# Performance work log

Measured on AMD Instinct MI355X. Metric: run time of the kernel, lower is better.

The kernel has to match this reference:

```python
import jax, jax.numpy as jnp
import numpy as np

GRAPH_SIZE = 96
ROWS = 5
COLS = 4
BATCH = 2048


def setup_inputs() -> dict:
    key = jax.random.key(0)
    k1, k2 = jax.random.split(key)
    x = jax.random.normal(k1, (BATCH, GRAPH_SIZE, GRAPH_SIZE), dtype=jnp.float32)
    # coef: nn.Parameter zeros -> kaiming_normal_, i.e. N(0, sqrt(2/fan_in)), fan_in=COLS
    coef = jax.random.normal(k2, (ROWS, COLS), dtype=jnp.float32) * np.float32(np.sqrt(2.0 / COLS))
    return {"x": x, "coef": coef}


def _acoef(x, coef):
    """Batched version of ACoef.forward.

    Per sample: t_i = trace(x^(i+2)) for i in [0, rows); scalar out =
    sum_{i,j} coef[i,j] * t_i^(j+1) / (G*G)^(i+j+1).
    """
    rows, cols = coef.shape
    G = x.shape[-1]
    xr = x.reshape(-1, G, G)  # [B, G, G]
    a = jnp.matmul(xr, xr)    # x^2 == a_series[0]
    traces = []
    for i in range(rows):
        traces.append(jnp.einsum('bii->b', a))  # trace(x^(i+2))
        if i < rows - 1:
            a = jnp.matmul(xr, a)  # advance to x^(i+3)
    t = jnp.stack(traces, axis=1)  # [B, rows]
    numel = jnp.float32(G * G)
    jexp = jnp.arange(1, cols + 1, dtype=jnp.float32)  # j+1
    iexp = jnp.arange(rows, dtype=jnp.float32)         # i
    denom = numel ** (iexp[:, None] + jexp[None, :])   # numel^(i+j+1), [rows, cols]
    ret = (t[:, :, None] ** jexp[None, None, :]) / denom  # [B, rows, cols]
    return jnp.sum(coef[None, :, :] * ret, axis=(1, 2))   # [B]


def reference(x, coef):
    return _acoef(x, coef)
```

## Files before the change

### kernel.cpp

```cpp
#include <hip/hip_runtime.h>
#include <stdint.h>

#define G 96
#define GS (G*G)
#define ST 104
#define ARR (G*ST)
#define NT 256

typedef short bf16x8  __attribute__((ext_vector_type(8)));
typedef short short4v __attribute__((ext_vector_type(4)));
typedef float f32x4   __attribute__((ext_vector_type(4)));

__device__ __forceinline__ short f2bf(float f) {
  uint32_t u = __builtin_bit_cast(uint32_t, f);
  u += 0x7FFFu + ((u >> 16) & 1u);
  return (short)(u >> 16);
}
__device__ __forceinline__ float bf2f(short s) {
  uint32_t u = ((uint32_t)(uint16_t)s) << 16;
  return __builtin_bit_cast(float, u);
}

__device__ __forceinline__ void mm_phase(const short* __restrict__ P,
                                         const short* __restrict__ Q,
                                         int wm, int wn, int lr, int lq,
                                         f32x4 acc[3][3]) {
  #pragma unroll
  for (int ks = 0; ks < 3; ++ks) {
    const int k0 = ks*32 + lq*8;
    bf16x8 af[3], bg[3];
    #pragma unroll
    for (int i = 0; i < 3; ++i)
      af[i] = *reinterpret_cast<const bf16x8*>(&P[(wm + i*16 + lr)*ST + k0]);
    #pragma unroll
    for (int j = 0; j < 3; ++j)
      bg[j] = *reinterpret_cast<const bf16x8*>(&Q[(wn + j*16 + lr)*ST + k0]);
    #pragma unroll
    for (int i = 0; i < 3; ++i)
      #pragma unroll
      for (int j = 0; j < 3; ++j)
        acc[i][j] = __builtin_amdgcn_mfma_f32_16x16x32_bf16(af[i], bg[j], acc[i][j], 0, 0, 0);
  }
}

__global__ __launch_bounds__(NT, 4) void acoef_kernel(
    const float* __restrict__ x, const float* __restrict__ coef,
    float* __restrict__ out) {
  __shared__ short sm[2*ARR];
  __shared__ float red[4][8];

  short* X  = sm;
  short* R1 = sm + ARR;

  const int tid  = threadIdx.x;
  const int b    = blockIdx.x;
  const int lane = tid & 63;
  const int w    = tid >> 6;
  const int wm   = (w >> 1) * 48;
  const int wn   = (w & 1)  * 48;
  const int lr   = lane & 15;
  const int lq   = lane >> 4;
  const int cr0  = lq * 4;

  const float* xg = x + (size_t)b * GS;
  #pragma unroll
  for (int it = 0; it < 9; ++it) {
    int f = tid + it*NT;
    float4 v = reinterpret_cast<const float4*>(xg)[f];
    int row = f / 24, c4 = (f - row*24) * 4;
    short4v sv = {f2bf(v.x), f2bf(v.y), f2bf(v.z), f2bf(v.w)};
    *reinterpret_cast<short4v*>(&X[row*ST + c4]) = sv;
  }
  __syncthreads();

  #pragma unroll
  for (int it = 0; it < 9; ++it) {
    int u  = tid + it*NT;
    int r2 = u % 96, cb = (u / 96) * 4;
    short4v sv = { X[(cb+0)*ST + r2], X[(cb+1)*ST + r2],
                   X[(cb+2)*ST + r2], X[(cb+3)*ST + r2] };
    *reinterpret_cast<short4v*>(&R1[r2*ST + cb]) = sv;
  }
  __syncthreads();

  f32x4 acc[3][3];
  #pragma unroll
  for (int i=0;i<3;i++)
    #pragma unroll
    for (int j=0;j<3;j++) acc[i][j] = (f32x4){0.f,0.f,0.f,0.f};
  mm_phase(X, R1, wm, wn, lr, lq, acc);

  float t0 = 0.f;
  #pragma unroll
  for (int i = 0; i < 3; ++i)
    #pragma unroll
    for (int j = 0; j < 3; ++j) {
      const int row0 = wm + i*16 + cr0, col = wn + j*16 + lr;
      #pragma unroll
      for (int r = 0; r < 4; ++r)
        if (row0 + r == col) t0 += acc[i][j][r];
    }
  __syncthreads();

  #pragma unroll
  for (int i = 0; i < 3; ++i)
    #pragma unroll
    for (int j = 0; j < 3; ++j) {
      const int row0 = wm + i*16 + cr0, col = wn + j*16 + lr;
      short4v sv = {f2bf(acc[i][j][0]), f2bf(acc[i][j][1]),
                    f2bf(acc[i][j][2]), f2bf(acc[i][j][3])};
      *reinterpret_cast<short4v*>(&R1[col*ST + row0]) = sv;
    }
  __syncthreads();

  f32x4 a2[3][3];
  #pragma unroll
  for (int i=0;i<3;i++)
    #pragma unroll
    for (int j=0;j<3;j++) a2[i][j] = (f32x4){0.f,0.f,0.f,0.f};
  mm_phase(R1, X, wm, wn, lr, lq, a2);

  float t1=0.f, t2=0.f, t3=0.f, t4=0.f;
  #pragma unroll
  for (int i = 0; i < 3; ++i)
    #pragma unroll
    for (int j = 0; j < 3; ++j) {
      const int row0 = wm + i*16 + cr0, col = wn + j*16 + lr;
      short4v ar = *reinterpret_cast<const short4v*>(&R1[col*ST + row0]);
      #pragma unroll
      for (int r = 0; r < 4; ++r) {
        float wv = a2[i][j][r];
        if (row0 + r == col) t1 += wv;
        t2 += wv * bf2f(X[(row0+r)*ST + col]);
        t3 += wv * bf2f(ar[r]);
      }
    }
  __syncthreads();

  #pragma unroll
  for (int i = 0; i < 3; ++i)
    #pragma unroll
    for (int j = 0; j < 3; ++j) {
      const int row0 = wm + i*16 + cr0, col = wn + j*16 + lr;
      short4v sv = {f2bf(a2[i][j][0]), f2bf(a2[i][j][1]),
                    f2bf(a2[i][j][2]), f2bf(a2[i][j][3])};
      *reinterpret_cast<short4v*>(&R1[col*ST + row0]) = sv;
    }
  __syncthreads();

  #pragma unroll
  for (int i = 0; i < 3; ++i)
    #pragma unroll
    for (int j = 0; j < 3; ++j) {
      const int row0 = wm + i*16 + cr0, col = wn + j*16 + lr;
      #pragma unroll
      for (int r = 0; r < 4; ++r)
        t4 += a2[i][j][r] * bf2f(R1[(row0+r)*ST + col]);
    }

  #pragma unroll
  for (int off = 32; off > 0; off >>= 1) {
    t0 += __shfl_down(t0, off, 64);
    t1 += __shfl_down(t1, off, 64);
    t2 += __shfl_down(t2, off, 64);
    t3 += __shfl_down(t3, off, 64);
    t4 += __shfl_down(t4, off, 64);
  }
  if (lane == 0) {
    red[w][0]=t0; red[w][1]=t1; red[w][2]=t2; red[w][3]=t3; red[w][4]=t4;
  }
  __syncthreads();
  if (tid == 0) {
    float T[5];
    #pragma unroll
    for (int k = 0; k < 5; ++k) T[k] = red[0][k]+red[1][k]+red[2][k]+red[3][k];
    const float inv = 1.0f / (float)GS;
    float o = 0.f, pi = 1.f;
    #pragma unroll
    for (int i = 0; i < 5; ++i) {
      float u = T[i] * inv;
      float up = u;
      #pragma unroll
      for (int j = 0; j < 4; ++j) { o += coef[i*4+j] * up * pi; up *= u; }
      pi *= inv;
    }
    out[b] = o;
  }
}

extern "C" void kernel_launch(void* const* d_in, const int* in_sizes, int n_in,
                              void* d_out, int out_size, void* d_ws, size_t ws_size,
                              hipStream_t stream) {
  const float* x    = (const float*)d_in[0];
  const float* coef = (const float*)d_in[1];
  float* out        = (float*)d_out;
  const int batch   = in_sizes[0] / GS;
  acoef_kernel<<<batch, NT, 0, stream>>>(x, coef, out);
}
```

Measured before the change: 28.69 us.

## Compute transposed power products with extra MFMAs instead of LDS round-trips

Trace terms are now computed as elementwise products of fp32 MFMA accumulators and their transposes, e.g. trace(X^4)=sum(A∘A^T). This needs X^2 transposed and X^3 transposed, each obtained by an additional matmul. It removes one LDS store/sync round and the scattered bf16 LDS reads in the epilogues, and the extra operands stay in fp32 rather than bf16. The cost is roughly double the MFMA work and more live accumulator registers, which may add register pressure at the requested occupancy.

After: 38.92 us. +35.7%, slower.

```diff
diff --git a/kernel.cpp b/kernel.cpp
--- a/kernel.cpp
+++ b/kernel.cpp
@@ -16,10 +16,6 @@
   u += 0x7FFFu + ((u >> 16) & 1u);
   return (short)(u >> 16);
 }
-__device__ __forceinline__ float bf2f(short s) {
-  uint32_t u = ((uint32_t)(uint16_t)s) << 16;
-  return __builtin_bit_cast(float, u);
-}
 
 __device__ __forceinline__ void mm_phase(const short* __restrict__ P,
                                          const short* __restrict__ Q,
@@ -42,6 +38,11 @@
         acc[i][j] = __builtin_amdgcn_mfma_f32_16x16x32_bf16(af[i], bg[j], acc[i][j], 0, 0, 0);
   }
 }
+
+#define ZERO9(A) do { \
+  _Pragma("unroll") for (int i_=0;i_<3;i_++) \
+    _Pragma("unroll") for (int j_=0;j_<3;j_++) A[i_][j_] = (f32x4){0.f,0.f,0.f,0.f}; \
+} while (0)
 
 __global__ __launch_bounds__(NT, 4) void acoef_kernel(
     const float* __restrict__ x, const float* __restrict__ coef,
@@ -83,22 +84,53 @@
   }
   __syncthreads();
 
-  f32x4 acc[3][3];
-  #pragma unroll
-  for (int i=0;i<3;i++)
-    #pragma unroll
-    for (int j=0;j<3;j++) acc[i][j] = (f32x4){0.f,0.f,0.f,0.f};
-  mm_phase(X, R1, wm, wn, lr, lq, acc);
-
-  float t0 = 0.f;
+  f32x4 accA[3][3], accAT[3][3];
+  ZERO9(accA); ZERO9(accAT);
+  #pragma unroll
+  for (int ks = 0; ks < 3; ++ks) {
+    const int k0 = ks*32 + lq*8;
+    {
+      bf16x8 af[3], bg[3];
+      #pragma unroll
+      for (int i = 0; i < 3; ++i)
+        af[i] = *reinterpret_cast<const bf16x8*>(&X [(wm + i*16 + lr)*ST + k0]);
+      #pragma unroll
+      for (int j = 0; j < 3; ++j)
+        bg[j] = *reinterpret_cast<const bf16x8*>(&R1[(wn + j*16 + lr)*ST + k0]);
+      #pragma unroll
+      for (int i = 0; i < 3; ++i)
+        #pragma unroll
+        for (int j = 0; j < 3; ++j)
+          accA[i][j] = __builtin_amdgcn_mfma_f32_16x16x32_bf16(af[i], bg[j], accA[i][j], 0, 0, 0);
+    }
+    {
+      bf16x8 af[3], bg[3];
+      #pragma unroll
+      for (int i = 0; i < 3; ++i)
+        af[i] = *reinterpret_cast<const bf16x8*>(&R1[(wm + i*16 + lr)*ST + k0]);
+      #pragma unroll
+      for (int j = 0; j < 3; ++j)
+        bg[j] = *reinterpret_cast<const bf16x8*>(&X [(wn + j*16 + lr)*ST + k0]);
+      #pragma unroll
+      for (int i = 0; i < 3; ++i)
+        #pragma unroll
+        for (int j = 0; j < 3; ++j)
+          accAT[i][j] = __builtin_amdgcn_mfma_f32_16x16x32_bf16(af[i], bg[j], accAT[i][j], 0, 0, 0);
+    }
+  }
+
+  float t0 = 0.f, t2 = 0.f;
   #pragma unroll
   for (int i = 0; i < 3; ++i)
     #pragma unroll
     for (int j = 0; j < 3; ++j) {
       const int row0 = wm + i*16 + cr0, col = wn + j*16 + lr;
       #pragma unroll
-      for (int r = 0; r < 4; ++r)
-        if (row0 + r == col) t0 += acc[i][j][r];
+      for (int r = 0; r < 4; ++r) {
+        float a = accA[i][j][r];
+        if (row0 + r == col) t0 += a;
+        t2 += a * accAT[i][j][r];
+      }
     }
   __syncthreads();
 
@@ -107,56 +139,42 @@
     #pragma unroll
     for (int j = 0; j < 3; ++j) {
       const int row0 = wm + i*16 + cr0, col = wn + j*16 + lr;
-      short4v sv = {f2bf(acc[i][j][0]), f2bf(acc[i][j][1]),
-                    f2bf(acc[i][j][2]), f2bf(acc[i][j][3])};
+      short4v sv = {f2bf(accA[i][j][0]), f2bf(accA[i][j][1]),
+                    f2bf(accA[i][j][2]), f2bf(accA[i][j][3])};
       *reinterpret_cast<short4v*>(&R1[col*ST + row0]) = sv;
     }
   __syncthreads();
 
-  f32x4 a2[3][3];
-  #pragma unroll
-  for (int i=0;i<3;i++)
-    #pragma unroll
-    for (int j=0;j<3;j++) a2[i][j] = (f32x4){0.f,0.f,0.f,0.f};
-  mm_phase(R1, X, wm, wn, lr, lq, a2);
-
-  float t1=0.f, t2=0.f, t3=0.f, t4=0.f;
+  f32x4 accB3[3][3];
+  ZERO9(accB3);
+  mm_phase(X, R1, wm, wn, lr, lq, accB3);
+
+  float t1 = 0.f, t3 = 0.f;
   #pragma unroll
   for (int i = 0; i < 3; ++i)
     #pragma unroll
     for (int j = 0; j < 3; ++j) {
       const int row0 = wm + i*16 + cr0, col = wn + j*16 + lr;
-      short4v ar = *reinterpret_cast<const short4v*>(&R1[col*ST + row0]);
       #pragma unroll
       for (int r = 0; r < 4; ++r) {
-        float wv = a2[i][j][r];
-        if (row0 + r == col) t1 += wv;
-        t2 += wv * bf2f(X[(row0+r)*ST + col]);
-        t3 += wv * bf2f(ar[r]);
+        float v = accB3[i][j][r];
+        if (row0 + r == col) t1 += v;
+        t3 += accAT[i][j][r] * v;
       }
     }
-  __syncthreads();
-
-  #pragma unroll
-  for (int i = 0; i < 3; ++i)
-    #pragma unroll
-    for (int j = 0; j < 3; ++j) {
-      const int row0 = wm + i*16 + cr0, col = wn + j*16 + lr;
-      short4v sv = {f2bf(a2[i][j][0]), f2bf(a2[i][j][1]),
-                    f2bf(a2[i][j][2]), f2bf(a2[i][j][3])};
-      *reinterpret_cast<short4v*>(&R1[col*ST + row0]) = sv;
-    }
-  __syncthreads();
-
-  #pragma unroll
-  for (int i = 0; i < 3; ++i)
-    #pragma unroll
-    for (int j = 0; j < 3; ++j) {
-      const int row0 = wm + i*16 + cr0, col = wn + j*16 + lr;
+
+  f32x4 accB3T[3][3];
+  ZERO9(accB3T);
+  mm_phase(R1, X, wm, wn, lr, lq, accB3T);
+
+  float t4 = 0.f;
+  #pragma unroll
+  for (int i = 0; i < 3; ++i)
+    #pragma unroll
+    for (int j = 0; j < 3; ++j)
       #pragma unroll
       for (int r = 0; r < 4; ++r)
-        t4 += a2[i][j][r] * bf2f(R1[(row0+r)*ST + col]);
-    }
+        t4 += accB3[i][j][r] * accB3T[i][j][r];
 
   #pragma unroll
   for (int off = 32; off > 0; off >>= 1) {
```

## Restructure trace chain to compute x^4 by a third matmul and reuse x^2

Applied to the files above, without the earlier changes.

The kernel now runs three MFMA matmul phases instead of two. It forms x^2 and x^3, then writes x^2 back into the X buffer and multiplies again to get x^4 directly. tr(x^4) is taken from the diagonal of that product, and tr(x^5) and tr(x^6) come from elementwise products with the cached transposed x^2 fragments kept in registers. This drops the separate writeback of x^3 and its reload. In exchange it adds a full extra 96x96 matmul, which likely also changes rounding behaviour. The coefficient table is also staged into shared memory at block start.

New measurement: 31.48 us. 1.1x slower.

```diff
diff --git a/kernel.cpp b/kernel.cpp
--- a/kernel.cpp
+++ b/kernel.cpp
@@ -43,11 +43,17 @@
   }
 }
 
+#define ZERO9(A) do { \
+  _Pragma("unroll") for (int i_=0;i_<3;i_++) \
+    _Pragma("unroll") for (int j_=0;j_<3;j_++) A[i_][j_] = (f32x4){0.f,0.f,0.f,0.f}; \
+} while (0)
+
 __global__ __launch_bounds__(NT, 4) void acoef_kernel(
     const float* __restrict__ x, const float* __restrict__ coef,
     float* __restrict__ out) {
   __shared__ short sm[2*ARR];
   __shared__ float red[4][8];
+  __shared__ float cf[20];
 
   short* X  = sm;
   short* R1 = sm + ARR;
@@ -62,6 +68,8 @@
   const int lq   = lane >> 4;
   const int cr0  = lq * 4;
 
+  if (tid < 20) cf[tid] = coef[tid];
+
   const float* xg = x + (size_t)b * GS;
   #pragma unroll
   for (int it = 0; it < 9; ++it) {
@@ -83,12 +91,9 @@
   }
   __syncthreads();
 
-  f32x4 acc[3][3];
-  #pragma unroll
-  for (int i=0;i<3;i++)
-    #pragma unroll
-    for (int j=0;j<3;j++) acc[i][j] = (f32x4){0.f,0.f,0.f,0.f};
-  mm_phase(X, R1, wm, wn, lr, lq, acc);
+  f32x4 accA[3][3];
+  ZERO9(accA);
+  mm_phase(X, R1, wm, wn, lr, lq, accA);
 
   float t0 = 0.f;
   #pragma unroll
@@ -98,64 +103,77 @@
       const int row0 = wm + i*16 + cr0, col = wn + j*16 + lr;
       #pragma unroll
       for (int r = 0; r < 4; ++r)
-        if (row0 + r == col) t0 += acc[i][j][r];
-    }
-  __syncthreads();
-
-  #pragma unroll
-  for (int i = 0; i < 3; ++i)
-    #pragma unroll
-    for (int j = 0; j < 3; ++j) {
-      const int row0 = wm + i*16 + cr0, col = wn + j*16 + lr;
-      short4v sv = {f2bf(acc[i][j][0]), f2bf(acc[i][j][1]),
-                    f2bf(acc[i][j][2]), f2bf(acc[i][j][3])};
+        if (row0 + r == col) t0 += accA[i][j][r];
+    }
+  __syncthreads();
+
+  #pragma unroll
+  for (int i = 0; i < 3; ++i)
+    #pragma unroll
+    for (int j = 0; j < 3; ++j) {
+      const int row0 = wm + i*16 + cr0, col = wn + j*16 + lr;
+      short4v sv = {f2bf(accA[i][j][0]), f2bf(accA[i][j][1]),
+                    f2bf(accA[i][j][2]), f2bf(accA[i][j][3])};
       *reinterpret_cast<short4v*>(&R1[col*ST + row0]) = sv;
     }
   __syncthreads();
 
-  f32x4 a2[3][3];
-  #pragma unroll
-  for (int i=0;i<3;i++)
-    #pragma unroll
-    for (int j=0;j<3;j++) a2[i][j] = (f32x4){0.f,0.f,0.f,0.f};
-  mm_phase(R1, X, wm, wn, lr, lq, a2);
-
-  float t1=0.f, t2=0.f, t3=0.f, t4=0.f;
-  #pragma unroll
-  for (int i = 0; i < 3; ++i)
-    #pragma unroll
-    for (int j = 0; j < 3; ++j) {
-      const int row0 = wm + i*16 + cr0, col = wn + j*16 + lr;
-      short4v ar = *reinterpret_cast<const short4v*>(&R1[col*ST + row0]);
+  f32x4 accB3[3][3];
+  ZERO9(accB3);
+  mm_phase(X, R1, wm, wn, lr, lq, accB3);
+
+  float t1 = 0.f;
+  #pragma unroll
+  for (int i = 0; i < 3; ++i)
+    #pragma unroll
+    for (int j = 0; j < 3; ++j) {
+      const int row0 = wm + i*16 + cr0, col = wn + j*16 + lr;
+      #pragma unroll
+      for (int r = 0; r < 4; ++r)
+        if (row0 + r == col) t1 += accB3[i][j][r];
+    }
+  __syncthreads();
+
+  #pragma unroll
+  for (int i = 0; i < 3; ++i)
+    #pragma unroll
+    for (int j = 0; j < 3; ++j) {
+      const int row0 = wm + i*16 + cr0, col = wn + j*16 + lr;
+      #pragma unroll
+      for (int r = 0; r < 4; ++r)
+        X[(row0+r)*ST + col] = f2bf(accA[i][j][r]);
+    }
+  __syncthreads();
+
+  short4v pr[3][3];
+  float t3 = 0.f;
+  #pragma unroll
+  for (int i = 0; i < 3; ++i)
+    #pragma unroll
+    for (int j = 0; j < 3; ++j) {
+      const int row0 = wm + i*16 + cr0, col = wn + j*16 + lr;
+      pr[i][j] = *reinterpret_cast<const short4v*>(&X[col*ST + row0]);
+      #pragma unroll
+      for (int r = 0; r < 4; ++r)
+        t3 += accB3[i][j][r] * bf2f(pr[i][j][r]);
+    }
+
+  f32x4 accA2[3][3];
+  ZERO9(accA2);
+  mm_phase(X, R1, wm, wn, lr, lq, accA2);
+
+  float t2 = 0.f, t4 = 0.f;
+  #pragma unroll
+  for (int i = 0; i < 3; ++i)
+    #pragma unroll
+    for (int j = 0; j < 3; ++j) {
+      const int row0 = wm + i*16 + cr0, col = wn + j*16 + lr;
       #pragma unroll
       for (int r = 0; r < 4; ++r) {
-        float wv = a2[i][j][r];
-        if (row0 + r == col) t1 += wv;
-        t2 += wv * bf2f(X[(row0+r)*ST + col]);
-        t3 += wv * bf2f(ar[r]);
+        float v = accA2[i][j][r];
+        if (row0 + r == col) t2 += v;
+        t4 += v * bf2f(pr[i][j][r]);
       }
-    }
-  __syncthreads();
-
-  #pragma unroll
-  for (int i = 0; i < 3; ++i)
-    #pragma unroll
-    for (int j = 0; j < 3; ++j) {
-      const int row0 = wm + i*16 + cr0, col = wn + j*16 + lr;
-      short4v sv = {f2bf(a2[i][j][0]), f2bf(a2[i][j][1]),
-                    f2bf(a2[i][j][2]), f2bf(a2[i][j][3])};
-      *reinterpret_cast<short4v*>(&R1[col*ST + row0]) = sv;
-    }
-  __syncthreads();
-
-  #pragma unroll
-  for (int i = 0; i < 3; ++i)
-    #pragma unroll
-    for (int j = 0; j < 3; ++j) {
-      const int row0 = wm + i*16 + cr0, col = wn + j*16 + lr;
-      #pragma unroll
-      for (int r = 0; r < 4; ++r)
-        t4 += a2[i][j][r] * bf2f(R1[(row0+r)*ST + col]);
     }
 
   #pragma unroll
@@ -181,7 +199,7 @@
       float u = T[i] * inv;
       float up = u;
       #pragma unroll
-      for (int j = 0; j < 4; ++j) { o += coef[i*4+j] * up * pi; up *= u; }
+      for (int j = 0; j < 4; ++j) { o += cf[i*4+j] * up * pi; up *= u; }
       pi *= inv;
     }
     out[b] = o;
```

## Halve block to two waves and keep matrix powers in packed registers

Applied to the files above, without the earlier changes.

Shrinks each block from four waves to two, so each wave computes a 48x96 output strip with 18 MFMA accumulators. Intermediate powers stay in registers as packed bf16, so the trace products (the elementwise dot products) no longer need LDS round-trips. This takes four matmul phases instead of two, and X is loaded with 8-element vector stores. The aim is to cut LDS traffic and barriers, at the cost of twice the MFMA work, higher register pressure and fewer threads per block.

Result: slower. 79.28 us (+176.4%).

```diff
diff --git a/kernel.cpp b/kernel.cpp
--- a/kernel.cpp
+++ b/kernel.cpp
@@ -5,49 +5,60 @@
 #define GS (G*G)
 #define ST 104
 #define ARR (G*ST)
-#define NT 256
+#define NT 128
 
 typedef short bf16x8  __attribute__((ext_vector_type(8)));
-typedef short short4v __attribute__((ext_vector_type(4)));
 typedef float f32x4   __attribute__((ext_vector_type(4)));
+typedef uint32_t u32x2 __attribute__((ext_vector_type(2)));
 
 __device__ __forceinline__ short f2bf(float f) {
   uint32_t u = __builtin_bit_cast(uint32_t, f);
   u += 0x7FFFu + ((u >> 16) & 1u);
   return (short)(u >> 16);
 }
-__device__ __forceinline__ float bf2f(short s) {
-  uint32_t u = ((uint32_t)(uint16_t)s) << 16;
-  return __builtin_bit_cast(float, u);
-}
-
-__device__ __forceinline__ void mm_phase(const short* __restrict__ P,
-                                         const short* __restrict__ Q,
-                                         int wm, int wn, int lr, int lq,
-                                         f32x4 acc[3][3]) {
+__device__ __forceinline__ uint32_t pk2(float a, float b) {
+  return (uint32_t)(uint16_t)f2bf(a) | ((uint32_t)(uint16_t)f2bf(b) << 16);
+}
+__device__ __forceinline__ float unlo(uint32_t u) {
+  return __builtin_bit_cast(float, u << 16);
+}
+__device__ __forceinline__ float unhi(uint32_t u) {
+  return __builtin_bit_cast(float, u & 0xffff0000u);
+}
+
+__device__ __forceinline__ void mm_v7(const short* __restrict__ P,
+                                      const short* __restrict__ Q,
+                                      int wm, int lr, int lq,
+                                      f32x4 acc[3][6]) {
   #pragma unroll
   for (int ks = 0; ks < 3; ++ks) {
     const int k0 = ks*32 + lq*8;
-    bf16x8 af[3], bg[3];
+    bf16x8 af[3], bg[6];
     #pragma unroll
     for (int i = 0; i < 3; ++i)
       af[i] = *reinterpret_cast<const bf16x8*>(&P[(wm + i*16 + lr)*ST + k0]);
     #pragma unroll
-    for (int j = 0; j < 3; ++j)
-      bg[j] = *reinterpret_cast<const bf16x8*>(&Q[(wn + j*16 + lr)*ST + k0]);
+    for (int j = 0; j < 6; ++j)
+      bg[j] = *reinterpret_cast<const bf16x8*>(&Q[(j*16 + lr)*ST + k0]);
     #pragma unroll
     for (int i = 0; i < 3; ++i)
       #pragma unroll
-      for (int j = 0; j < 3; ++j)
+      for (int j = 0; j < 6; ++j)
         acc[i][j] = __builtin_amdgcn_mfma_f32_16x16x32_bf16(af[i], bg[j], acc[i][j], 0, 0, 0);
   }
 }
 
-__global__ __launch_bounds__(NT, 4) void acoef_kernel(
+#define ZERO18(A) do { \
+  _Pragma("unroll") for (int i_=0;i_<3;i_++) \
+    _Pragma("unroll") for (int j_=0;j_<6;j_++) A[i_][j_] = (f32x4){0.f,0.f,0.f,0.f}; \
+} while (0)
+
+__global__ __launch_bounds__(NT, 2) void acoef_kernel(
     const float* __restrict__ x, const float* __restrict__ coef,
     float* __restrict__ out) {
   __shared__ short sm[2*ARR];
-  __shared__ float red[4][8];
+  __shared__ float red[2][8];
+  __shared__ float cf[20];
 
   short* X  = sm;
   short* R1 = sm + ARR;
@@ -56,107 +67,113 @@
   const int b    = blockIdx.x;
   const int lane = tid & 63;
   const int w    = tid >> 6;
-  const int wm   = (w >> 1) * 48;
-  const int wn   = (w & 1)  * 48;
+  const int wm   = w * 48;
   const int lr   = lane & 15;
   const int lq   = lane >> 4;
   const int cr0  = lq * 4;
 
+  if (tid < 20) cf[tid] = coef[tid];
+
   const float* xg = x + (size_t)b * GS;
   #pragma unroll
   for (int it = 0; it < 9; ++it) {
-    int f = tid + it*NT;
-    float4 v = reinterpret_cast<const float4*>(xg)[f];
-    int row = f / 24, c4 = (f - row*24) * 4;
-    short4v sv = {f2bf(v.x), f2bf(v.y), f2bf(v.z), f2bf(v.w)};
-    *reinterpret_cast<short4v*>(&X[row*ST + c4]) = sv;
-  }
-  __syncthreads();
-
-  #pragma unroll
-  for (int it = 0; it < 9; ++it) {
+    int c = tid + it*NT;
+    float4 v0 = reinterpret_cast<const float4*>(xg)[2*c];
+    float4 v1 = reinterpret_cast<const float4*>(xg)[2*c+1];
+    int row = c / 12, col8 = (c - row*12) * 8;
+    bf16x8 sv = { f2bf(v0.x), f2bf(v0.y), f2bf(v0.z), f2bf(v0.w),
+                  f2bf(v1.x), f2bf(v1.y), f2bf(v1.z), f2bf(v1.w) };
+    *reinterpret_cast<bf16x8*>(&X[row*ST + col8]) = sv;
+  }
+  __syncthreads();
+
+  #pragma unroll
+  for (int it = 0; it < 18; ++it) {
     int u  = tid + it*NT;
     int r2 = u % 96, cb = (u / 96) * 4;
-    short4v sv = { X[(cb+0)*ST + r2], X[(cb+1)*ST + r2],
-                   X[(cb+2)*ST + r2], X[(cb+3)*ST + r2] };
-    *reinterpret_cast<short4v*>(&R1[r2*ST + cb]) = sv;
-  }
-  __syncthreads();
-
-  f32x4 acc[3][3];
-  #pragma unroll
-  for (int i=0;i<3;i++)
-    #pragma unroll
-    for (int j=0;j<3;j++) acc[i][j] = (f32x4){0.f,0.f,0.f,0.f};
-  mm_phase(X, R1, wm, wn, lr, lq, acc);
+    uint32_t p0 = pk2(0.f, 0.f), p1 = p0;
+    short s0 = X[(cb+0)*ST + r2], s1 = X[(cb+1)*ST + r2];
+    short s2 = X[(cb+2)*ST + r2], s3 = X[(cb+3)*ST + r2];
+    p0 = (uint32_t)(uint16_t)s0 | ((uint32_t)(uint16_t)s1 << 16);
+    p1 = (uint32_t)(uint16_t)s2 | ((uint32_t)(uint16_t)s3 << 16);
+    u32x2 pv = {p0, p1};
+    *reinterpret_cast<u32x2*>(&R1[r2*ST + cb]) = pv;
+  }
+  __syncthreads();
+
+  f32x4 acc[3][6];
+  ZERO18(acc);
+  mm_v7(X, R1, wm, lr, lq, acc);
 
   float t0 = 0.f;
-  #pragma unroll
-  for (int i = 0; i < 3; ++i)
-    #pragma unroll
-    for (int j = 0; j < 3; ++j) {
-      const int row0 = wm + i*16 + cr0, col = wn + j*16 + lr;
+  uint32_t pkA[3][6][2];
+  #pragma unroll
+  for (int i = 0; i < 3; ++i)
+    #pragma unroll
+    for (int j = 0; j < 6; ++j) {
+      const int row0 = wm + i*16 + cr0, col = j*16 + lr;
       #pragma unroll
       for (int r = 0; r < 4; ++r)
         if (row0 + r == col) t0 += acc[i][j][r];
-    }
-  __syncthreads();
-
-  #pragma unroll
-  for (int i = 0; i < 3; ++i)
-    #pragma unroll
-    for (int j = 0; j < 3; ++j) {
-      const int row0 = wm + i*16 + cr0, col = wn + j*16 + lr;
-      short4v sv = {f2bf(acc[i][j][0]), f2bf(acc[i][j][1]),
-                    f2bf(acc[i][j][2]), f2bf(acc[i][j][3])};
-      *reinterpret_cast<short4v*>(&R1[col*ST + row0]) = sv;
-    }
-  __syncthreads();
-
-  f32x4 a2[3][3];
-  #pragma unroll
-  for (int i=0;i<3;i++)
-    #pragma unroll
-    for (int j=0;j<3;j++) a2[i][j] = (f32x4){0.f,0.f,0.f,0.f};
-  mm_phase(R1, X, wm, wn, lr, lq, a2);
-
-  float t1=0.f, t2=0.f, t3=0.f, t4=0.f;
-  #pragma unroll
-  for (int i = 0; i < 3; ++i)
-    #pragma unroll
-    for (int j = 0; j < 3; ++j) {
-      const int row0 = wm + i*16 + cr0, col = wn + j*16 + lr;
-      short4v ar = *reinterpret_cast<const short4v*>(&R1[col*ST + row0]);
-      #pragma unroll
-      for (int r = 0; r < 4; ++r) {
-        float wv = a2[i][j][r];
-        if (row0 + r == col) t1 += wv;
-        t2 += wv * bf2f(X[(row0+r)*ST + col]);
-        t3 += wv * bf2f(ar[r]);
-      }
-    }
-  __syncthreads();
-
-  #pragma unroll
-  for (int i = 0; i < 3; ++i)
-    #pragma unroll
-    for (int j = 0; j < 3; ++j) {
-      const int row0 = wm + i*16 + cr0, col = wn + j*16 + lr;
-      short4v sv = {f2bf(a2[i][j][0]), f2bf(a2[i][j][1]),
-                    f2bf(a2[i][j][2]), f2bf(a2[i][j][3])};
-      *reinterpret_cast<short4v*>(&R1[col*ST + row0]) = sv;
-    }
-  __syncthreads();
-
-  #pragma unroll
-  for (int i = 0; i < 3; ++i)
-    #pragma unroll
-    for (int j = 0; j < 3; ++j) {
-      const int row0 = wm + i*16 + cr0, col = wn + j*16 + lr;
+      pkA[i][j][0] = pk2(acc[i][j][0], acc[i][j][1]);
+      pkA[i][j][1] = pk2(acc[i][j][2], acc[i][j][3]);
+    }
+
+  ZERO18(acc);
+  mm_v7(R1, X, wm, lr, lq, acc);
+
+  float t2 = 0.f;
+  uint32_t pkAT[3][6][2];
+  #pragma unroll
+  for (int i = 0; i < 3; ++i)
+    #pragma unroll
+    for (int j = 0; j < 6; ++j) {
+      t2 += unlo(pkA[i][j][0]) * acc[i][j][0] + unhi(pkA[i][j][0]) * acc[i][j][1]
+          + unlo(pkA[i][j][1]) * acc[i][j][2] + unhi(pkA[i][j][1]) * acc[i][j][3];
+      pkAT[i][j][0] = pk2(acc[i][j][0], acc[i][j][1]);
+      pkAT[i][j][1] = pk2(acc[i][j][2], acc[i][j][3]);
+    }
+  __syncthreads();
+
+  #pragma unroll
+  for (int i = 0; i < 3; ++i)
+    #pragma unroll
+    for (int j = 0; j < 6; ++j) {
+      const int row0 = wm + i*16 + cr0, col = j*16 + lr;
+      u32x2 pv = {pkA[i][j][0], pkA[i][j][1]};
+      *reinterpret_cast<u32x2*>(&R1[col*ST + row0]) = pv;
+    }
+  __syncthreads();
+
+  ZERO18(acc);
+  mm_v7(X, R1, wm, lr, lq, acc);
+
+  float t1 = 0.f, t3 = 0.f;
+  uint32_t pkB[3][6][2];
+  #pragma unroll
+  for (int i = 0; i < 3; ++i)
+    #pragma unroll
+    for (int j = 0; j < 6; ++j) {
+      const int row0 = wm + i*16 + cr0, col = j*16 + lr;
       #pragma unroll
       for (int r = 0; r < 4; ++r)
-        t4 += a2[i][j][r] * bf2f(R1[(row0+r)*ST + col]);
-    }
+        if (row0 + r == col) t1 += acc[i][j][r];
+      t3 += unlo(pkAT[i][j][0]) * acc[i][j][0] + unhi(pkAT[i][j][0]) * acc[i][j][1]
+          + unlo(pkAT[i][j][1]) * acc[i][j][2] + unhi(pkAT[i][j][1]) * acc[i][j][3];
+      pkB[i][j][0] = pk2(acc[i][j][0], acc[i][j][1]);
+      pkB[i][j][1] = pk2(acc[i][j][2], acc[i][j][3]);
+    }
+
+  ZERO18(acc);
+  mm_v7(R1, X, wm, lr, lq, acc);
+
+  float t4 = 0.f;
+  #pragma unroll
+  for (int i = 0; i < 3; ++i)
+    #pragma unroll
+    for (int j = 0; j < 6; ++j)
+      t4 += unlo(pkB[i][j][0]) * acc[i][j][0] + unhi(pkB[i][j][0]) * acc[i][j][1]
+          + unlo(pkB[i][j][1]) * acc[i][j][2] + unhi(pkB[i][j][1]) * acc[i][j][3];
 
   #pragma unroll
   for (int off = 32; off > 0; off >>= 1) {
@@ -173,7 +190,7 @@
   if (tid == 0) {
     float T[5];
     #pragma unroll
-    for (int k = 0; k < 5; ++k) T[k] = red[0][k]+red[1][k]+red[2][k]+red[3][k];
+    for (int k = 0; k < 5; ++k) T[k] = red[0][k] + red[1][k];
     const float inv = 1.0f / (float)GS;
     float o = 0.f, pi = 1.f;
     #pragma unroll
@@ -181,7 +198,7 @@
       float u = T[i] * inv;
       float up = u;
       #pragma unroll
-      for (int j = 0; j < 4; ++j) { o += coef[i*4+j] * up * pi; up *= u; }
+      for (int j = 0; j < 4; ++j) { o += cf[i*4+j] * up * pi; up *= u; }
       pi *= inv;
     }
     out[b] = o;
```
